# Performance work log

Measured on AMD Instinct MI355X. Metric: run time of the kernel, lower is better.

The kernel has to match this reference:

```python
import jax, jax.numpy as jnp
import numpy as np

B, A, D = 64, 4096, 512
TOP_K = 5

def setup_inputs() -> dict:
    key = jax.random.key(0)
    k1, k2, k3 = jax.random.split(key, 3)
    s_embed = jax.random.normal(k1, (B, D), dtype=jnp.float32)
    a_embeds = jax.random.normal(k2, (B, A, D), dtype=jnp.float32)
    available_mask = jax.random.randint(k3, (B, A), 0, 2) > 0
    # make sure each row has at least one available action
    available_mask = available_mask.at[:, 0].set(True)
    return {"s_embed": s_embed, "a_embeds": a_embeds,
            "available_mask": available_mask, "alpha": 1}


def reference(s_embed, a_embeds, available_mask, alpha):
    alpha = jnp.float32(alpha)
    # logits[b,a] = <s_embed[b], a_embeds[b,a]>
    logits = jnp.einsum('bd,bad->ba', s_embed, a_embeds)  # [B, A]
    # masked_fill unavailable actions with (global min - 1)
    fill = jnp.min(logits) - 1.0
    logits = jnp.where(available_mask, logits, fill)
    # top-k mask via scatter
    k = min(logits.shape[1], TOP_K)
    _, top_ids = jax.lax.top_k(logits, k)  # [B, k]
    rows = jnp.arange(logits.shape[0])[:, None]
    top_mask = jnp.zeros(logits.shape, dtype=bool).at[rows, top_ids].set(True)
    # temperature softmax (max-shifted, matching the torch code)
    probs = jax.nn.softmax((logits - jnp.max(logits, -1, keepdims=True)) / alpha, axis=-1)
    # keep only available & top-k, renormalize
    keep = available_mask & top_mask
    probs = jnp.where(keep, probs, 0.0)
    probs = probs / jnp.sum(probs, -1, keepdims=True)
    # categorical sample (zeros -> -inf logits, never sampled)
    action = jax.random.categorical(jax.random.key(42), jnp.log(probs), axis=-1)
    return action, logits
```

## Files before the change

### kernel.cpp

```cpp
#include <hip/hip_runtime.h>
#include <cstdint>
#include <cstddef>

#define NB 64
#define NA 4096
#define ND 512

__device__ __forceinline__ unsigned enc_f(float f){
  unsigned b = __float_as_uint(f);
  return (b & 0x80000000u) ? ~b : (b | 0x80000000u);
}
__device__ __forceinline__ float dec_f(unsigned e){
  unsigned b = (e & 0x80000000u) ? (e ^ 0x80000000u) : ~e;
  return __uint_as_float(b);
}

__device__ __forceinline__ unsigned rotl32(unsigned x, int d){ return (x << d) | (x >> (32 - d)); }

__device__ unsigned threefry_bits(unsigned n){
  const unsigned ks0 = 0u;
  const unsigned ks1 = 42u;
  const unsigned ks2 = 0x1BD11BDAu ^ ks0 ^ ks1;
  unsigned x0 = 0u;
  unsigned x1 = n;
  x0 += ks0; x1 += ks1;
  const int r0[4] = {13, 15, 26, 6};
  const int r1[4] = {17, 29, 16, 24};
  #pragma unroll
  for (int j = 0; j < 4; j++){ x0 += x1; x1 = rotl32(x1, r0[j]); x1 ^= x0; }
  x0 += ks1; x1 += ks2 + 1u;
  #pragma unroll
  for (int j = 0; j < 4; j++){ x0 += x1; x1 = rotl32(x1, r1[j]); x1 ^= x0; }
  x0 += ks2; x1 += ks0 + 2u;
  #pragma unroll
  for (int j = 0; j < 4; j++){ x0 += x1; x1 = rotl32(x1, r0[j]); x1 ^= x0; }
  x0 += ks0; x1 += ks1 + 3u;
  #pragma unroll
  for (int j = 0; j < 4; j++){ x0 += x1; x1 = rotl32(x1, r1[j]); x1 ^= x0; }
  x0 += ks1; x1 += ks2 + 4u;
  #pragma unroll
  for (int j = 0; j < 4; j++){ x0 += x1; x1 = rotl32(x1, r0[j]); x1 ^= x0; }
  x0 += ks2; x1 += ks0 + 5u;
  return x0 ^ x1;
}

__global__ void init_ws(unsigned* ws){ ws[threadIdx.x * 16] = 0xFFFFFFFFu; }

__global__ __launch_bounds__(256) void dot_kernel(const float* __restrict__ s,
                                                  const float* __restrict__ ae,
                                                  float* __restrict__ logits,
                                                  unsigned* __restrict__ minw){
  __shared__ unsigned sm[4];
  int wave = threadIdx.x >> 6;
  int lane = threadIdx.x & 63;
  int blk  = blockIdx.x;
  int b = blk >> 10;
  int a = ((blk & 1023) << 2) | wave;
  const float* ar = ae + (size_t)(b * NA + a) * ND;
  const float* sr = s + b * ND;
  float4 a0 = *(const float4*)(ar + lane * 4);
  float4 a1 = *(const float4*)(ar + 256 + lane * 4);
  float4 s0 = *(const float4*)(sr + lane * 4);
  float4 s1 = *(const float4*)(sr + 256 + lane * 4);
  float p = a0.x*s0.x + a0.y*s0.y + a0.z*s0.z + a0.w*s0.w
          + a1.x*s1.x + a1.y*s1.y + a1.z*s1.z + a1.w*s1.w;
  #pragma unroll
  for (int off = 32; off > 0; off >>= 1) p += __shfl_xor(p, off, 64);
  if (lane == 0){
    logits[(size_t)b * NA + a] = p;
    sm[wave] = enc_f(p);
  }
  __syncthreads();
  if (threadIdx.x == 0){
    unsigned m01 = sm[0] < sm[1] ? sm[0] : sm[1];
    unsigned m23 = sm[2] < sm[3] ? sm[2] : sm[3];
    unsigned m   = m01 < m23 ? m01 : m23;
    atomicMin(minw + (blk & 255) * 16, m);
  }
}

__global__ __launch_bounds__(256) void row_kernel(float* __restrict__ out,
                                                  const void* __restrict__ maskp,
                                                  const unsigned* __restrict__ ws,
                                                  const unsigned* __restrict__ alpha_raw){
  __shared__ float row[NA];
  __shared__ unsigned su[4];
  __shared__ float rv[4]; __shared__ int ri[4];
  __shared__ float selv[5]; __shared__ int seli[5];
  __shared__ int s_mflag;
  __shared__ float s_fill;
  int b = blockIdx.x;
  int t = threadIdx.x;
  float* lrow = out + NB + (size_t)b * NA;
  const unsigned char* m8  = (const unsigned char*)maskp;
  const unsigned*      m32 = (const unsigned*)maskp;

  if (t == 0) s_mflag = 1;
  __syncthreads();
  for (int i = t; i < 4096; i += 256)
    if (m32[i] > 1u) s_mflag = 0;

  unsigned e = ws[t * 16];
  #pragma unroll
  for (int off = 32; off > 0; off >>= 1){
    unsigned o = __shfl_xor(e, off, 64);
    e = o < e ? o : e;
  }
  if ((t & 63) == 0) su[t >> 6] = e;
  __syncthreads();
  if (t == 0){
    unsigned r01 = su[0] < su[1] ? su[0] : su[1];
    unsigned r23 = su[2] < su[3] ? su[2] : su[3];
    unsigned r   = r01 < r23 ? r01 : r23;
    s_fill = dec_f(r) - 1.0f;
  }
  __syncthreads();
  int   mflag = s_mflag;
  float fill  = s_fill;

  for (int a = t; a < NA; a += 256){
    int idx = b * NA + a;
    bool av = mflag ? (m32[idx] != 0u) : (m8[idx] != 0);
    float v = lrow[a];
    float mv = av ? v : fill;
    row[a]  = mv;
    lrow[a] = mv;
  }
  __syncthreads();

  for (int k = 0; k < 5; k++){
    float bv = -INFINITY; int bi = 0x7FFFFFFF;
    for (int a = t; a < NA; a += 256){
      float v = row[a];
      if (v > bv){ bv = v; bi = a; }
    }
    #pragma unroll
    for (int off = 32; off > 0; off >>= 1){
      float ov = __shfl_xor(bv, off, 64);
      int   oi = __shfl_xor(bi, off, 64);
      if (ov > bv || (ov == bv && oi < bi)){ bv = ov; bi = oi; }
    }
    if ((t & 63) == 0){ rv[t >> 6] = bv; ri[t >> 6] = bi; }
    __syncthreads();
    if (t == 0){
      float fv = rv[0]; int fi = ri[0];
      for (int w = 1; w < 4; w++)
        if (rv[w] > fv || (rv[w] == fv && ri[w] < fi)){ fv = rv[w]; fi = ri[w]; }
      selv[k] = fv; seli[k] = fi;
      row[fi] = -INFINITY;
    }
    __syncthreads();
  }

  if (t == 0){
    unsigned ab = *alpha_raw;
    float alpha = (ab < 0x00800000u) ? (float)(int)ab : __uint_as_float(ab);
    float best = -INFINITY; int ba = 0;
    for (int k = 0; k < 5; k++){
      int idx  = seli[k];
      int gidx = b * NA + idx;
      bool av = mflag ? (m32[gidx] != 0u) : (m8[gidx] != 0);
      if (!av) continue;
      unsigned bits = threefry_bits((unsigned)gidx);
      float f = __uint_as_float((bits >> 9) | 0x3F800000u) - 1.0f;
      const float tiny = 1.17549435e-38f;
      float u = fmaxf(tiny, f + tiny);
      float g = -logf(-logf(u));
      float sc = selv[k] / alpha + g;
      if (sc > best){ best = sc; ba = idx; }
    }
    out[b] = (float)ba;
  }
}

extern "C" void kernel_launch(void* const* d_in, const int* in_sizes, int n_in,
                              void* d_out, int out_size, void* d_ws, size_t ws_size,
                              hipStream_t stream){
  const float*    s     = (const float*)d_in[0];
  const float*    ae    = (const float*)d_in[1];
  const void*     mask  = d_in[2];
  const unsigned* alpha = (const unsigned*)d_in[3];
  float*    out = (float*)d_out;
  unsigned* ws  = (unsigned*)d_ws;

  hipLaunchKernelGGL(init_ws,    dim3(1),           dim3(256), 0, stream, ws);
  hipLaunchKernelGGL(dot_kernel, dim3(NB * NA / 4), dim3(256), 0, stream, s, ae, out + NB, ws);
  hipLaunchKernelGGL(row_kernel, dim3(NB),          dim3(256), 0, stream, out, mask, ws, alpha);
}
```

Baseline: 125.2 us.

## Compute four logits per wave and replace atomic min with per-block buffer

Each wave now computes four action dot products instead of one, so the state vector load is reused and each block issues more loads in flight. The grid shrinks fourfold. The global min is now written as one float per block into a workspace buffer and reduced in the row kernel, which removes the atomicMin, the float encoding and the init kernel launch. In exchange, every one of the 64 row blocks has to scan all 16384 partial minima, and each thread holds more registers.

```diff
diff --git a/kernel.cpp b/kernel.cpp
--- a/kernel.cpp
+++ b/kernel.cpp
@@ -5,15 +5,6 @@
 #define NB 64
 #define NA 4096
 #define ND 512
-
-__device__ __forceinline__ unsigned enc_f(float f){
-  unsigned b = __float_as_uint(f);
-  return (b & 0x80000000u) ? ~b : (b | 0x80000000u);
-}
-__device__ __forceinline__ float dec_f(unsigned e){
-  unsigned b = (e & 0x80000000u) ? (e ^ 0x80000000u) : ~e;
-  return __uint_as_float(b);
-}
 
 __device__ __forceinline__ unsigned rotl32(unsigned x, int d){ return (x << d) | (x >> (32 - d)); }
 
@@ -44,47 +35,59 @@
   return x0 ^ x1;
 }
 
-__global__ void init_ws(unsigned* ws){ ws[threadIdx.x * 16] = 0xFFFFFFFFu; }
-
 __global__ __launch_bounds__(256) void dot_kernel(const float* __restrict__ s,
                                                   const float* __restrict__ ae,
                                                   float* __restrict__ logits,
-                                                  unsigned* __restrict__ minw){
-  __shared__ unsigned sm[4];
+                                                  float* __restrict__ minbuf){
+  __shared__ float sm[4];
   int wave = threadIdx.x >> 6;
   int lane = threadIdx.x & 63;
   int blk  = blockIdx.x;
-  int b = blk >> 10;
-  int a = ((blk & 1023) << 2) | wave;
-  const float* ar = ae + (size_t)(b * NA + a) * ND;
+  int b     = blk >> 8;
+  int abase = ((blk & 255) << 4) | (wave << 2);
   const float* sr = s + b * ND;
-  float4 a0 = *(const float4*)(ar + lane * 4);
-  float4 a1 = *(const float4*)(ar + 256 + lane * 4);
   float4 s0 = *(const float4*)(sr + lane * 4);
   float4 s1 = *(const float4*)(sr + 256 + lane * 4);
-  float p = a0.x*s0.x + a0.y*s0.y + a0.z*s0.z + a0.w*s0.w
-          + a1.x*s1.x + a1.y*s1.y + a1.z*s1.z + a1.w*s1.w;
+  const float* ar = ae + ((size_t)(b * NA) + abase) * ND + lane * 4;
+  float4 a00 = *(const float4*)(ar);
+  float4 a01 = *(const float4*)(ar + 256);
+  float4 a10 = *(const float4*)(ar + 512);
+  float4 a11 = *(const float4*)(ar + 768);
+  float4 a20 = *(const float4*)(ar + 1024);
+  float4 a21 = *(const float4*)(ar + 1280);
+  float4 a30 = *(const float4*)(ar + 1536);
+  float4 a31 = *(const float4*)(ar + 1792);
+  float p0 = a00.x*s0.x + a00.y*s0.y + a00.z*s0.z + a00.w*s0.w
+           + a01.x*s1.x + a01.y*s1.y + a01.z*s1.z + a01.w*s1.w;
+  float p1 = a10.x*s0.x + a10.y*s0.y + a10.z*s0.z + a10.w*s0.w
+           + a11.x*s1.x + a11.y*s1.y + a11.z*s1.z + a11.w*s1.w;
+  float p2 = a20.x*s0.x + a20.y*s0.y + a20.z*s0.z + a20.w*s0.w
+           + a21.x*s1.x + a21.y*s1.y + a21.z*s1.z + a21.w*s1.w;
+  float p3 = a30.x*s0.x + a30.y*s0.y + a30.z*s0.z + a30.w*s0.w
+           + a31.x*s1.x + a31.y*s1.y + a31.z*s1.z + a31.w*s1.w;
   #pragma unroll
-  for (int off = 32; off > 0; off >>= 1) p += __shfl_xor(p, off, 64);
+  for (int off = 32; off > 0; off >>= 1){
+    p0 += __shfl_xor(p0, off, 64);
+    p1 += __shfl_xor(p1, off, 64);
+    p2 += __shfl_xor(p2, off, 64);
+    p3 += __shfl_xor(p3, off, 64);
+  }
   if (lane == 0){
-    logits[(size_t)b * NA + a] = p;
-    sm[wave] = enc_f(p);
+    float4 v = make_float4(p0, p1, p2, p3);
+    *(float4*)(logits + (size_t)b * NA + abase) = v;
+    sm[wave] = fminf(fminf(p0, p1), fminf(p2, p3));
   }
   __syncthreads();
-  if (threadIdx.x == 0){
-    unsigned m01 = sm[0] < sm[1] ? sm[0] : sm[1];
-    unsigned m23 = sm[2] < sm[3] ? sm[2] : sm[3];
-    unsigned m   = m01 < m23 ? m01 : m23;
-    atomicMin(minw + (blk & 255) * 16, m);
-  }
+  if (threadIdx.x == 0)
+    minbuf[blk] = fminf(fminf(sm[0], sm[1]), fminf(sm[2], sm[3]));
 }
 
 __global__ __launch_bounds__(256) void row_kernel(float* __restrict__ out,
                                                   const void* __restrict__ maskp,
-                                                  const unsigned* __restrict__ ws,
+                                                  const float* __restrict__ minbuf,
                                                   const unsigned* __restrict__ alpha_raw){
   __shared__ float row[NA];
-  __shared__ unsigned su[4];
+  __shared__ float su[4];
   __shared__ float rv[4]; __shared__ int ri[4];
   __shared__ float selv[5]; __shared__ int seli[5];
   __shared__ int s_mflag;
@@ -100,20 +103,14 @@
   for (int i = t; i < 4096; i += 256)
     if (m32[i] > 1u) s_mflag = 0;
 
-  unsigned e = ws[t * 16];
+  float e = minbuf[t];
+  for (int i = t + 256; i < 16384; i += 256) e = fminf(e, minbuf[i]);
   #pragma unroll
-  for (int off = 32; off > 0; off >>= 1){
-    unsigned o = __shfl_xor(e, off, 64);
-    e = o < e ? o : e;
-  }
+  for (int off = 32; off > 0; off >>= 1) e = fminf(e, __shfl_xor(e, off, 64));
   if ((t & 63) == 0) su[t >> 6] = e;
   __syncthreads();
-  if (t == 0){
-    unsigned r01 = su[0] < su[1] ? su[0] : su[1];
-    unsigned r23 = su[2] < su[3] ? su[2] : su[3];
-    unsigned r   = r01 < r23 ? r01 : r23;
-    s_fill = dec_f(r) - 1.0f;
-  }
+  if (t == 0)
+    s_fill = fminf(fminf(su[0], su[1]), fminf(su[2], su[3])) - 1.0f;
   __syncthreads();
   int   mflag = s_mflag;
   float fill  = s_fill;
@@ -180,10 +177,9 @@
   const float*    ae    = (const float*)d_in[1];
   const void*     mask  = d_in[2];
   const unsigned* alpha = (const unsigned*)d_in[3];
-  float*    out = (float*)d_out;
-  unsigned* ws  = (unsigned*)d_ws;
+  float* out = (float*)d_out;
+  float* ws  = (float*)d_ws;
 
-  hipLaunchKernelGGL(init_ws,    dim3(1),           dim3(256), 0, stream, ws);
-  hipLaunchKernelGGL(dot_kernel, dim3(NB * NA / 4), dim3(256), 0, stream, s, ae, out + NB, ws);
-  hipLaunchKernelGGL(row_kernel, dim3(NB),          dim3(256), 0, stream, out, mask, ws, alpha);
+  hipLaunchKernelGGL(dot_kernel, dim3(NB * NA / 16), dim3(256), 0, stream, s, ae, out + NB, ws);
+  hipLaunchKernelGGL(row_kernel, dim3(NB),           dim3(256), 0, stream, out, mask, ws, alpha);
 }
```

After: 130.7 us. 1.04x slower.
